# Kernel tuning notes

Measured on AMD Instinct MI355X. Metric: run time of the kernel, lower is better.

The kernel has to match this reference:

```python
import jax, jax.numpy as jnp
import numpy as np

B, A, V, D = 16, 1024, 512, 512
TEMPERATURE = 1.0
NEG = jnp.float32(-1e30)  # stand-in for -inf (avoids inf-inf NaNs in grads)
EPS = 1e-12               # F.normalize eps


def setup_inputs() -> dict:
    key = jax.random.key(0)
    k1, k2, k3 = jax.random.split(key, 3)
    audio_features = jax.random.normal(k1, (B, A, D), jnp.float32)
    video_features = jax.random.normal(k2, (B, V, D), jnp.float32)
    W = jax.random.normal(k3, (D, D), jnp.float32) / np.sqrt(D)  # nn.Linear weight [out,in]
    b = jnp.zeros((D,), jnp.float32)
    return {"audio_features": audio_features, "video_features": video_features, "W": W, "b": b}


def _normalize(x):
    n = jnp.linalg.norm(x, axis=-1, keepdims=True)
    return x / jnp.maximum(n, EPS)


def _dtw_score(sim):
    # sim: [B, A, V]. dp[i,j] = sim[i-1,j-1] + max(dp[i-1,j], dp[i,j-1], dp[i-1,j-1]).
    Bn, An, Vn = sim.shape
    init_row = jnp.full((Bn, Vn + 1), NEG).at[:, 0].set(0.0)  # dp row 0

    def row_step(prev_row, cost_row):
        # prev_row: [B, V+1], cost_row: [B, V]
        def col_step(left, xs):
            c, up, diag = xs  # each [B]
            val = c + jnp.maximum(jnp.maximum(up, left), diag)
            return val, val

        xs = (cost_row.T, prev_row[:, 1:].T, prev_row[:, :-1].T)  # [V, B] each
        _, vals = jax.lax.scan(col_step, jnp.full((Bn,), NEG), xs)  # vals: [V, B]
        new_row = jnp.concatenate([jnp.full((Bn, 1), NEG), vals.T], axis=1)
        return new_row, None

    final_row, _ = jax.lax.scan(row_step, init_row, jnp.swapaxes(sim, 0, 1))
    return final_row[:, -1]  # dp[:, A, V]


def reference(audio_features, video_features, W, b):
    audio_proj = jnp.einsum('bad,ed->bae', audio_features, W) + b
    video_proj = jnp.einsum('bvd,ed->bve', video_features, W) + b
    a_n = _normalize(audio_proj)
    v_n = _normalize(video_proj)
    similarity = jnp.einsum('bad,bvd->bav', a_n, v_n) / TEMPERATURE  # [B, A, V]
    alignment_score = _dtw_score(similarity)                          # [B]
    path_prob = jax.nn.softmax(similarity, axis=-1)
    aligned_video = jnp.einsum('bav,bvd->bad', path_prob, video_features)  # [B, A, D]
    return aligned_video, alignment_score
```

## Files before the change

### kernel.cpp

```cpp
#include <hip/hip_runtime.h>
#include <math.h>

#define B_DIM 16
#define A_DIM 1024
#define V_DIM 512
#define D_DIM 512
#define NEGV  (-1e30f)

typedef short bf16x8 __attribute__((ext_vector_type(8)));
typedef float floatx4 __attribute__((ext_vector_type(4)));

__device__ __forceinline__ short bf16_rne(float f) {
    unsigned u = __float_as_uint(f);
    return (short)((u + 0x7fffu + ((u >> 16) & 1u)) >> 16);
}

__device__ __forceinline__ float max3f(float a, float b, float c) {
    float d;
    asm("v_max3_f32 %0, %1, %2, %3" : "=v"(d) : "v"(a), "v"(b), "v"(c));
    return d;
}

__global__ __launch_bounds__(256) void cvt3_bf16_kernel(
    const float* __restrict__ in0, unsigned short* __restrict__ out0, int nb0,
    const float* __restrict__ in1, unsigned short* __restrict__ out1, int nb1,
    const float* __restrict__ in2, unsigned short* __restrict__ out2)
{
    int blk = blockIdx.x;
    const float* in; unsigned short* out;
    if (blk < nb0)              { in = in0; out = out0; }
    else if (blk < nb0 + nb1)   { in = in1; out = out1; blk -= nb0; }
    else                        { in = in2; out = out2; blk -= nb0 + nb1; }
    const int i = blk * 256 + threadIdx.x;
    float4 u = ((const float4*)in)[2*i];
    float4 v = ((const float4*)in)[2*i + 1];
    bf16x8 h;
    h[0]=bf16_rne(u.x); h[1]=bf16_rne(u.y); h[2]=bf16_rne(u.z); h[3]=bf16_rne(u.w);
    h[4]=bf16_rne(v.x); h[5]=bf16_rne(v.y); h[6]=bf16_rne(v.z); h[7]=bf16_rne(v.w);
    *(bf16x8*)(out + (size_t)i * 8) = h;
}

__global__ __launch_bounds__(256) void gemm_bf16_nt(
    const unsigned short* __restrict__ Ag, const unsigned short* __restrict__ Bg,
    const float* __restrict__ bias, float* __restrict__ Cg,
    int M, int N, int K, size_t strA, size_t strB, size_t strC)
{
    __shared__ __align__(16) unsigned short lA[8*64*8];
    __shared__ __align__(16) unsigned short lB[8*64*8];

    const unsigned short* Ab = Ag + (size_t)blockIdx.z * strA;
    const unsigned short* Bb = Bg + (size_t)blockIdx.z * strB;
    float*                Cb = Cg + (size_t)blockIdx.z * strC;

    const int m0 = blockIdx.y * 128;
    const int n0 = blockIdx.x * 128;
    const int tid = threadIdx.x, lane = tid & 63;
    const int w = tid >> 6, wy = w >> 1, wx = w & 1;

    const int u0 = tid, u1 = tid + 256;
    const int r_u0 = ((u0 >> 6) << 4) + (u0 & 15), k_u0 = ((u0 >> 4) & 3) * 8;
    const int r_u1 = ((u1 >> 6) << 4) + (u1 & 15), k_u1 = ((u1 >> 4) & 3) * 8;

    const unsigned short* gA0 = Ab + (size_t)(m0 + r_u0) * K + k_u0;
    const unsigned short* gA1 = Ab + (size_t)(m0 + r_u1) * K + k_u1;
    const unsigned short* gB0 = Bb + (size_t)(n0 + r_u0) * K + k_u0;
    const unsigned short* gB1 = Bb + (size_t)(n0 + r_u1) * K + k_u1;

    floatx4 acc[4][4];
    #pragma unroll
    for (int i = 0; i < 4; ++i)
        #pragma unroll
        for (int j = 0; j < 4; ++j) acc[i][j] = (floatx4){0.f, 0.f, 0.f, 0.f};

    bf16x8 a0 = *(const bf16x8*)(gA0);
    bf16x8 a1 = *(const bf16x8*)(gA1);
    bf16x8 b0 = *(const bf16x8*)(gB0);
    bf16x8 b1 = *(const bf16x8*)(gB1);

    for (int k0 = 0; k0 < K; k0 += 32) {
        __syncthreads();
        *(bf16x8*)&lA[(size_t)u0 * 8] = a0;
        *(bf16x8*)&lA[(size_t)u1 * 8] = a1;
        *(bf16x8*)&lB[(size_t)u0 * 8] = b0;
        *(bf16x8*)&lB[(size_t)u1 * 8] = b1;
        __syncthreads();

        if (k0 + 32 < K) {
            a0 = *(const bf16x8*)(gA0 + k0 + 32);
            a1 = *(const bf16x8*)(gA1 + k0 + 32);
            b0 = *(const bf16x8*)(gB0 + k0 + 32);
            b1 = *(const bf16x8*)(gB1 + k0 + 32);
        }

        bf16x8 fa[4], fb[4];
        #pragma unroll
        for (int t = 0; t < 4; ++t) {
            fa[t] = *(const bf16x8*)&lA[(((wy*4 + t)*64) + lane) * 8];
            fb[t] = *(const bf16x8*)&lB[(((wx*4 + t)*64) + lane) * 8];
        }
        #pragma unroll
        for (int i = 0; i < 4; ++i)
            #pragma unroll
            for (int j = 0; j < 4; ++j)
                acc[i][j] = __builtin_amdgcn_mfma_f32_16x16x32_bf16(fa[i], fb[j], acc[i][j], 0, 0, 0);
    }

    const int q = lane >> 4, c = lane & 15;
    #pragma unroll
    for (int i = 0; i < 4; ++i)
        #pragma unroll
        for (int j = 0; j < 4; ++j) {
            const int n = n0 + (wx*4 + j)*16 + c;
            const float bv = bias ? bias[n] : 0.f;
            #pragma unroll
            for (int r = 0; r < 4; ++r) {
                const int m = m0 + (wy*4 + i)*16 + q*4 + r;
                Cb[(size_t)m * N + n] = acc[i][j][r] + bv;
            }
        }
}

__global__ __launch_bounds__(256) void rownorm_cvt_kernel(
    const float* __restrict__ in, unsigned short* __restrict__ out)
{
    const int wave = threadIdx.x >> 6;
    const int lane = threadIdx.x & 63;
    const size_t r = (size_t)blockIdx.x * 4 + wave;
    const float* p = in + r * D_DIM + lane * 8;
    float4 u = *(const float4*)p;
    float4 w = *(const float4*)(p + 4);
    float ss = u.x*u.x + u.y*u.y + u.z*u.z + u.w*u.w
             + w.x*w.x + w.y*w.y + w.z*w.z + w.w*w.w;
    #pragma unroll
    for (int m = 1; m < 64; m <<= 1) ss += __shfl_xor(ss, m, 64);
    const float inv = 1.0f / fmaxf(sqrtf(ss), 1e-12f);
    bf16x8 h;
    h[0]=bf16_rne(u.x*inv); h[1]=bf16_rne(u.y*inv); h[2]=bf16_rne(u.z*inv); h[3]=bf16_rne(u.w*inv);
    h[4]=bf16_rne(w.x*inv); h[5]=bf16_rne(w.y*inv); h[6]=bf16_rne(w.z*inv); h[7]=bf16_rne(w.w*inv);
    *(bf16x8*)(out + r * D_DIM + lane * 8) = h;
}

template <int CTRL, int RMASK>
__device__ __forceinline__ float fdpp(float oldv, float src) {
    int r = __builtin_amdgcn_update_dpp(
        __float_as_int(oldv), __float_as_int(src), CTRL, RMASK, 0xF, false);
    return __int_as_float(r);
}

__global__ __launch_bounds__(256) void softmax_skew_kernel(
    const float* __restrict__ sim, unsigned short* __restrict__ Pbf,
    float* __restrict__ skew)
{
    const int wave = threadIdx.x >> 6;
    const int lane = threadIdx.x & 63;
    const size_t r = (size_t)blockIdx.x * 4 + wave;
    const float* p = sim + r * V_DIM + lane * 8;
    float4 u = *(const float4*)p;
    float4 w = *(const float4*)(p + 4);
    float s[8] = {u.x,u.y,u.z,u.w,w.x,w.y,w.z,w.w};

    float m = s[0];
    #pragma unroll
    for (int k = 1; k < 8; ++k) m = fmaxf(m, s[k]);
    #pragma unroll
    for (int t = 1; t < 64; t <<= 1) m = fmaxf(m, __shfl_xor(m, t, 64));

    const float L2E = 1.44269504f;
    float ex[8];
    float e = 0.f;
    #pragma unroll
    for (int k = 0; k < 8; ++k) { ex[k] = exp2f((s[k] - m) * L2E); e += ex[k]; }
    #pragma unroll
    for (int t = 1; t < 64; t <<= 1) e += __shfl_xor(e, t, 64);
    const float ri = 1.0f / e;

    bf16x8 h;
    #pragma unroll
    for (int k = 0; k < 8; ++k) h[k] = bf16_rne(ex[k] * ri);
    *(bf16x8*)(Pbf + r * V_DIM + lane * 8) = h;

    const int g  = ((int)r & 1023) >> 2;
    const int sh = (g & 63) + 72 * (g >> 6);
    float* Sk = skew + r * V_DIM;
    const int base = lane * 8 + sh;
    #pragma unroll
    for (int k = 0; k < 8; ++k) Sk[(base + k) & 511] = s[k];
}

__global__ __launch_bounds__(256) void transpose_cvt_kernel(
    const float* __restrict__ in, unsigned short* __restrict__ out)
{
    __shared__ float t[32][33];
    const int b = blockIdx.z;
    const int v0 = blockIdx.y * 32, d0 = blockIdx.x * 32;
    const int x = threadIdx.x & 31, y0 = (threadIdx.x >> 5) * 4;
    const float* I = in + ((size_t)b * V_DIM + v0) * D_DIM + d0;
    #pragma unroll
    for (int r = 0; r < 4; ++r) t[y0 + r][x] = I[(size_t)(y0 + r) * D_DIM + x];
    __syncthreads();
    unsigned short* O = out + ((size_t)b * D_DIM + d0) * V_DIM + v0;
    #pragma unroll
    for (int r = 0; r < 4; ++r) O[(size_t)(y0 + r) * V_DIM + x] = (unsigned short)bf16_rne(t[x][y0 + r]);
}

__global__ __launch_bounds__(256) void pv_dtw_kernel(
    const unsigned short* __restrict__ Pbf, const unsigned short* __restrict__ vTb,
    const float* __restrict__ skew, float* __restrict__ out_aligned,
    float* __restrict__ out_score)
{
    __shared__ __align__(16) unsigned short lA[8*64*8];
    __shared__ __align__(16) unsigned short lB[8*64*8];

    if (blockIdx.x < 16) {
        const int b    = blockIdx.x;
        const int tid  = threadIdx.x;
        const int lane = tid & 63;
        const int wv   = tid >> 6;
        const int off  = lane + 72 * wv;

        float* bndAll = (float*)lA;
        float* bndP = bndAll + wv * 520;
        const float* bndC = bndAll + (wv > 0 ? wv - 1 : 0) * 520;
        for (int i = tid; i < 3 * 520; i += 256) bndAll[i] = NEGV;
        __syncthreads();

        const float* R0 = skew + ((size_t)(b * 1024 + tid * 4)) * 512;
        const float* R1 = R0 + 512;
        const float* R2 = R0 + 1024;
        const float* R3 = R0 + 1536;

        float dp[4] = {NEGV, NEGV, NEGV, NEGV};
        float st[8];
        float upC = NEGV;
        float upL = (tid == 0) ? 0.0f : NEGV;

        float4 A0[4], A1[4], B0[4], B1[4];
        A0[0] = *(const float4*)(R0);      A1[0] = *(const float4*)(R0 + 4);
        A0[1] = *(const float4*)(R1);      A1[1] = *(const float4*)(R1 + 4);
        A0[2] = *(const float4*)(R2);      A1[2] = *(const float4*)(R2 + 4);
        A0[3] = *(const float4*)(R3);      A1[3] = *(const float4*)(R3 + 4);
        B0[0] = *(const float4*)(R0 + 8);  B1[0] = *(const float4*)(R0 + 12);
        B0[1] = *(const float4*)(R1 + 8);  B1[1] = *(const float4*)(R1 + 12);
        B0[2] = *(const float4*)(R2 + 8);  B1[2] = *(const float4*)(R2 + 12);
        B0[3] = *(const float4*)(R3 + 8);  B1[3] = *(const float4*)(R3 + 12);

#define DTW_STEP(K, CV0, CV1, CV2, CV3, FK)                                   \
        {                                                                     \
            const unsigned jj = (unsigned)(sb + (K) - off);                   \
            if (jj < 512u) {                                                  \
                float u = upC, g = upL, old, nd;                              \
                old = dp[0]; nd = (CV0) + max3f(u, dp[0], g); dp[0] = nd; g = old; u = nd; \
                old = dp[1]; nd = (CV1) + max3f(u, dp[1], g); dp[1] = nd; g = old; u = nd; \
                old = dp[2]; nd = (CV2) + max3f(u, dp[2], g); dp[2] = nd; g = old; u = nd; \
                old = dp[3]; nd = (CV3) + max3f(u, dp[3], g); dp[3] = nd;                  \
            }                                                                 \
            st[K] = dp[3];                                                    \
            upL = upC;                                                        \
            upC = fdpp<0x138, 0xF>((FK), dp[3]);                              \
        }

#define DTW_BATCH(C0, C1)                                                     \
        {                                                                     \
            float4 f0, f1;                                                    \
            const int ps = sb + 8 - 72 * wv;                                  \
            if (wv > 0 && ps >= 0 && ps <= 512) {                             \
                f0 = *(const float4*)&bndC[ps];                               \
                f1 = *(const float4*)&bndC[ps + 4];                           \
            } else {                                                          \
                f0 = make_float4(NEGV, NEGV, NEGV, NEGV); f1 = f0;            \
            }                                                                 \
            DTW_STEP(0, C0[0].x, C0[1].x, C0[2].x, C0[3].x, f0.x)             \
            DTW_STEP(1, C0[0].y, C0[1].y, C0[2].y, C0[3].y, f0.y)             \
            DTW_STEP(2, C0[0].z, C0[1].z, C0[2].z, C0[3].z, f0.z)             \
            DTW_STEP(3, C0[0].w, C0[1].w, C0[2].w, C0[3].w, f0.w)             \
            DTW_STEP(4, C1[0].x, C1[1].x, C1[2].x, C1[3].x, f1.x)             \
            DTW_STEP(5, C1[0].y, C1[1].y, C1[2].y, C1[3].y, f1.y)             \
            DTW_STEP(6, C1[0].z, C1[1].z, C1[2].z, C1[3].z, f1.z)             \
            DTW_STEP(7, C1[0].w, C1[1].w, C1[2].w, C1[3].w, f1.w)             \
            {                                                                 \
                const int o16 = (sb + 16) & 511;                              \
                C0[0] = *(const float4*)(R0 + o16); C1[0] = *(const float4*)(R0 + o16 + 4); \
                C0[1] = *(const float4*)(R1 + o16); C1[1] = *(const float4*)(R1 + o16 + 4); \
                C0[2] = *(const float4*)(R2 + o16); C1[2] = *(const float4*)(R2 + o16 + 4); \
                C0[3] = *(const float4*)(R3 + o16); C1[3] = *(const float4*)(R3 + o16 + 4); \
            }                                                                 \
            if (wv < 3 && lane == 63) {                                       \
                _Pragma("unroll")                                             \
                for (int k = 0; k < 8; ++k) {                                 \
                    const int jp = sb + k - 63 - 72 * wv;                     \
                    const int adr = ((unsigned)jp < 512u) ? (jp + 7) : 519;   \
                    bndP[adr] = st[k];                                        \
                }                                                             \
            }                                                                 \
            asm volatile("s_waitcnt lgkmcnt(0)" ::: "memory");                \
            __builtin_amdgcn_s_barrier();                                     \
            asm volatile("" ::: "memory");                                    \
        }

        #pragma unroll 1
        for (int bt = 0; bt < 100; bt += 2) {
            int sb = bt * 8;
            DTW_BATCH(A0, A1)
            sb += 8;
            DTW_BATCH(B0, B1)
        }
#undef DTW_BATCH
#undef DTW_STEP
        if (tid == 255) out_score[b] = dp[3];
        return;
    }

    const int bid = blockIdx.x - 16;
    const int n0 = (bid & 3) * 128;
    const int m0 = ((bid >> 2) & 7) * 128;
    const int bz = bid >> 5;
    const int K = V_DIM, N = D_DIM;

    const unsigned short* Ab = Pbf + (size_t)bz * A_DIM * V_DIM;
    const unsigned short* Bb = vTb + (size_t)bz * V_DIM * D_DIM;
    float*                Cb = out_aligned + (size_t)bz * A_DIM * D_DIM;

    const int tid = threadIdx.x, lane = tid & 63;
    const int w = tid >> 6, wy = w >> 1, wx = w & 1;
    const int u0 = tid, u1 = tid + 256;
    const int r_u0 = ((u0 >> 6) << 4) + (u0 & 15), k_u0 = ((u0 >> 4) & 3) * 8;
    const int r_u1 = ((u1 >> 6) << 4) + (u1 & 15), k_u1 = ((u1 >> 4) & 3) * 8;

    const unsigned short* gA0 = Ab + (size_t)(m0 + r_u0) * K + k_u0;
    const unsigned short* gA1 = Ab + (size_t)(m0 + r_u1) * K + k_u1;
    const unsigned short* gB0 = Bb + (size_t)(n0 + r_u0) * K + k_u0;
    const unsigned short* gB1 = Bb + (size_t)(n0 + r_u1) * K + k_u1;

    floatx4 acc[4][4];
    #pragma unroll
    for (int i = 0; i < 4; ++i)
        #pragma unroll
        for (int j = 0; j < 4; ++j) acc[i][j] = (floatx4){0.f, 0.f, 0.f, 0.f};

    bf16x8 a0 = *(const bf16x8*)(gA0);
    bf16x8 a1 = *(const bf16x8*)(gA1);
    bf16x8 b0 = *(const bf16x8*)(gB0);
    bf16x8 b1 = *(const bf16x8*)(gB1);

    for (int k0 = 0; k0 < K; k0 += 32) {
        __syncthreads();
        *(bf16x8*)&lA[(size_t)u0 * 8] = a0;
        *(bf16x8*)&lA[(size_t)u1 * 8] = a1;
        *(bf16x8*)&lB[(size_t)u0 * 8] = b0;
        *(bf16x8*)&lB[(size_t)u1 * 8] = b1;
        __syncthreads();
        if (k0 + 32 < K) {
            a0 = *(const bf16x8*)(gA0 + k0 + 32);
            a1 = *(const bf16x8*)(gA1 + k0 + 32);
            b0 = *(const bf16x8*)(gB0 + k0 + 32);
            b1 = *(const bf16x8*)(gB1 + k0 + 32);
        }
        bf16x8 fa[4], fb[4];
        #pragma unroll
        for (int t = 0; t < 4; ++t) {
            fa[t] = *(const bf16x8*)&lA[(((wy*4 + t)*64) + lane) * 8];
            fb[t] = *(const bf16x8*)&lB[(((wx*4 + t)*64) + lane) * 8];
        }
        #pragma unroll
        for (int i = 0; i < 4; ++i)
            #pragma unroll
            for (int j = 0; j < 4; ++j)
                acc[i][j] = __builtin_amdgcn_mfma_f32_16x16x32_bf16(fa[i], fb[j], acc[i][j], 0, 0, 0);
    }

    const int q = lane >> 4, c = lane & 15;
    #pragma unroll
    for (int i = 0; i < 4; ++i)
        #pragma unroll
        for (int j = 0; j < 4; ++j) {
            const int n = n0 + (wx*4 + j)*16 + c;
            #pragma unroll
            for (int r = 0; r < 4; ++r) {
                const int m = m0 + (wy*4 + i)*16 + q*4 + r;
                Cb[(size_t)m * N + n] = acc[i][j][r];
            }
        }
}

extern "C" void kernel_launch(void* const* d_in, const int* in_sizes, int n_in,
                              void* d_out, int out_size, void* d_ws, size_t ws_size,
                              hipStream_t stream)
{
    const float* audio = (const float*)d_in[0];
    const float* video = (const float*)d_in[1];
    const float* W     = (const float*)d_in[2];
    const float* bias  = (const float*)d_in[3];

    float* out_aligned = (float*)d_out;
    float* out_score   = (float*)d_out + (size_t)B_DIM * A_DIM * D_DIM;

    const size_t NA = (size_t)B_DIM * A_DIM * D_DIM;
    const size_t NV = (size_t)B_DIM * V_DIM * D_DIM;
    const size_t NS = (size_t)B_DIM * A_DIM * V_DIM;

    float* ws = (float*)d_ws;
    float*          a_p  = ws;
    float*          v_p  = a_p + NA;
    float*          sim  = v_p + NV;
    unsigned short* abf  = (unsigned short*)(sim + NS);
    unsigned short* vbf  = (unsigned short*)(sim + NS) + NA;
    unsigned short* v_nb = vbf + NV;
    unsigned short* Wbf  = v_nb + NV;
    unsigned short* a_nb = (unsigned short*)v_p;
    unsigned short* Pbf  = abf;
    unsigned short* vTb  = vbf;
    float*          skew = a_p;

    {
        const int nb_a = (int)(NA / 8 / 256);
        const int nb_v = (int)(NV / 8 / 256);
        const int nb_w = D_DIM * D_DIM / 8 / 256;
        cvt3_bf16_kernel<<<dim3(nb_a + nb_v + nb_w), dim3(256), 0, stream>>>(
            audio, abf, nb_a, video, vbf, nb_v, W, Wbf);
    }

    gemm_bf16_nt<<<dim3(D_DIM/128, (B_DIM*A_DIM)/128, 1), dim3(256), 0, stream>>>(
        abf, Wbf, bias, a_p, B_DIM*A_DIM, D_DIM, D_DIM, 0, 0, 0);
    gemm_bf16_nt<<<dim3(D_DIM/128, (B_DIM*V_DIM)/128, 1), dim3(256), 0, stream>>>(
        vbf, Wbf, bias, v_p, B_DIM*V_DIM, D_DIM, D_DIM, 0, 0, 0);

    rownorm_cvt_kernel<<<dim3((B_DIM*V_DIM)/4), dim3(256), 0, stream>>>(v_p, v_nb);
    rownorm_cvt_kernel<<<dim3((B_DIM*A_DIM)/4), dim3(256), 0, stream>>>(a_p, a_nb);

    gemm_bf16_nt<<<dim3(V_DIM/128, A_DIM/128, B_DIM), dim3(256), 0, stream>>>(
        a_nb, v_nb, nullptr, sim, A_DIM, V_DIM, D_DIM,
        (size_t)A_DIM*D_DIM, (size_t)V_DIM*D_DIM, (size_t)A_DIM*V_DIM);

    transpose_cvt_kernel<<<dim3(D_DIM/32, V_DIM/32, B_DIM), dim3(256), 0, stream>>>(video, vTb);

    softmax_skew_kernel<<<dim3((B_DIM*A_DIM)/4), dim3(256), 0, stream>>>(sim, Pbf, skew);

    pv_dtw_kernel<<<dim3(16 + (D_DIM/128)*(A_DIM/128)*B_DIM), dim3(256), 0, stream>>>(
        Pbf, vTb, skew, out_aligned, out_score);
}
```

Before: 324.6 us.

## Transpose DTW cost layout for coalesced loads and merge projection/norm launches

Softmax now writes a column-major, skewed copy of the similarity matrix through shared memory. Each DTW thread then fetches four consecutive rows with one coalesced float4 per diagonal step instead of strided row reads. The two projection GEMMs are merged into one launch, and the two row-norm kernels plus the video transpose are merged into another, which reduces launch count and tail effects. A shared GEMM tile body is factored out. The skewed buffer is wider (768 columns), so there are extra writes, and softmax gains a shared-memory transpose step.

```diff
diff --git a/kernel.cpp b/kernel.cpp
--- a/kernel.cpp
+++ b/kernel.cpp
@@ -6,6 +6,7 @@
 #define V_DIM 512
 #define D_DIM 512
 #define NEGV  (-1e30f)
+#define SKT_W 768
 
 typedef short bf16x8 __attribute__((ext_vector_type(8)));
 typedef float floatx4 __attribute__((ext_vector_type(4)));
@@ -40,20 +41,12 @@
     *(bf16x8*)(out + (size_t)i * 8) = h;
 }
 
-__global__ __launch_bounds__(256) void gemm_bf16_nt(
-    const unsigned short* __restrict__ Ag, const unsigned short* __restrict__ Bg,
-    const float* __restrict__ bias, float* __restrict__ Cg,
-    int M, int N, int K, size_t strA, size_t strB, size_t strC)
-{
-    __shared__ __align__(16) unsigned short lA[8*64*8];
-    __shared__ __align__(16) unsigned short lB[8*64*8];
-
-    const unsigned short* Ab = Ag + (size_t)blockIdx.z * strA;
-    const unsigned short* Bb = Bg + (size_t)blockIdx.z * strB;
-    float*                Cb = Cg + (size_t)blockIdx.z * strC;
-
-    const int m0 = blockIdx.y * 128;
-    const int n0 = blockIdx.x * 128;
+__device__ __forceinline__ void gemm_tile_body(
+    const unsigned short* __restrict__ Ab, const unsigned short* __restrict__ Bb,
+    const float* __restrict__ bias, float* __restrict__ Cb,
+    int m0, int n0, int K, int N,
+    unsigned short* lA, unsigned short* lB)
+{
     const int tid = threadIdx.x, lane = tid & 63;
     const int w = tid >> 6, wy = w >> 1, wx = w & 1;
 
@@ -120,24 +113,73 @@
         }
 }
 
-__global__ __launch_bounds__(256) void rownorm_cvt_kernel(
-    const float* __restrict__ in, unsigned short* __restrict__ out)
-{
-    const int wave = threadIdx.x >> 6;
-    const int lane = threadIdx.x & 63;
-    const size_t r = (size_t)blockIdx.x * 4 + wave;
-    const float* p = in + r * D_DIM + lane * 8;
-    float4 u = *(const float4*)p;
-    float4 w = *(const float4*)(p + 4);
-    float ss = u.x*u.x + u.y*u.y + u.z*u.z + u.w*u.w
-             + w.x*w.x + w.y*w.y + w.z*w.z + w.w*w.w;
-    #pragma unroll
-    for (int m = 1; m < 64; m <<= 1) ss += __shfl_xor(ss, m, 64);
-    const float inv = 1.0f / fmaxf(sqrtf(ss), 1e-12f);
-    bf16x8 h;
-    h[0]=bf16_rne(u.x*inv); h[1]=bf16_rne(u.y*inv); h[2]=bf16_rne(u.z*inv); h[3]=bf16_rne(u.w*inv);
-    h[4]=bf16_rne(w.x*inv); h[5]=bf16_rne(w.y*inv); h[6]=bf16_rne(w.z*inv); h[7]=bf16_rne(w.w*inv);
-    *(bf16x8*)(out + r * D_DIM + lane * 8) = h;
+__global__ __launch_bounds__(256) void gemm_bf16_nt(
+    const unsigned short* __restrict__ Ag, const unsigned short* __restrict__ Bg,
+    const float* __restrict__ bias, float* __restrict__ Cg,
+    int M, int N, int K, size_t strA, size_t strB, size_t strC)
+{
+    __shared__ __align__(16) unsigned short lA[8*64*8];
+    __shared__ __align__(16) unsigned short lB[8*64*8];
+    const unsigned short* Ab = Ag + (size_t)blockIdx.z * strA;
+    const unsigned short* Bb = Bg + (size_t)blockIdx.z * strB;
+    float*                Cb = Cg + (size_t)blockIdx.z * strC;
+    gemm_tile_body(Ab, Bb, bias, Cb, blockIdx.y * 128, blockIdx.x * 128, K, N, lA, lB);
+}
+
+__global__ __launch_bounds__(256) void gemm_proj2(
+    const unsigned short* __restrict__ abf, const unsigned short* __restrict__ vbf,
+    const unsigned short* __restrict__ Wbf, const float* __restrict__ bias,
+    float* __restrict__ a_p, float* __restrict__ v_p)
+{
+    __shared__ __align__(16) unsigned short lA[8*64*8];
+    __shared__ __align__(16) unsigned short lB[8*64*8];
+    const int by = blockIdx.y;
+    const unsigned short* Ab; float* Cb; int m0;
+    if (by < 128) { Ab = abf; Cb = a_p; m0 = by * 128; }
+    else          { Ab = vbf; Cb = v_p; m0 = (by - 128) * 128; }
+    gemm_tile_body(Ab, Wbf, bias, Cb, m0, blockIdx.x * 128, D_DIM, D_DIM, lA, lB);
+}
+
+__global__ __launch_bounds__(256) void norm2_transpose_kernel(
+    const float* __restrict__ a_p, unsigned short* __restrict__ a_nb,
+    const float* __restrict__ v_p, unsigned short* __restrict__ v_nb,
+    const float* __restrict__ video, unsigned short* __restrict__ vTb)
+{
+    __shared__ float t[32][33];
+    const int bx = blockIdx.x;
+    if (bx < 6144) {
+        const float* in; unsigned short* out; int rb;
+        if (bx < 4096) { in = a_p; out = a_nb; rb = bx; }
+        else           { in = v_p; out = v_nb; rb = bx - 4096; }
+        const int wave = threadIdx.x >> 6;
+        const int lane = threadIdx.x & 63;
+        const size_t r = (size_t)rb * 4 + wave;
+        const float* p = in + r * D_DIM + lane * 8;
+        float4 u = *(const float4*)p;
+        float4 w = *(const float4*)(p + 4);
+        float ss = u.x*u.x + u.y*u.y + u.z*u.z + u.w*u.w
+                 + w.x*w.x + w.y*w.y + w.z*w.z + w.w*w.w;
+        #pragma unroll
+        for (int m = 1; m < 64; m <<= 1) ss += __shfl_xor(ss, m, 64);
+        const float inv = 1.0f / fmaxf(sqrtf(ss), 1e-12f);
+        bf16x8 h;
+        h[0]=bf16_rne(u.x*inv); h[1]=bf16_rne(u.y*inv); h[2]=bf16_rne(u.z*inv); h[3]=bf16_rne(u.w*inv);
+        h[4]=bf16_rne(w.x*inv); h[5]=bf16_rne(w.y*inv); h[6]=bf16_rne(w.z*inv); h[7]=bf16_rne(w.w*inv);
+        *(bf16x8*)(out + r * D_DIM + lane * 8) = h;
+    } else {
+        const int tt = bx - 6144;
+        const int d0 = (tt & 15) * 32;
+        const int v0 = ((tt >> 4) & 15) * 32;
+        const int b  = tt >> 8;
+        const int x = threadIdx.x & 31, y0 = (threadIdx.x >> 5) * 4;
+        const float* I = video + ((size_t)b * V_DIM + v0) * D_DIM + d0;
+        #pragma unroll
+        for (int r = 0; r < 4; ++r) t[y0 + r][x] = I[(size_t)(y0 + r) * D_DIM + x];
+        __syncthreads();
+        unsigned short* O = vTb + ((size_t)b * D_DIM + d0) * V_DIM + v0;
+        #pragma unroll
+        for (int r = 0; r < 4; ++r) O[(size_t)(y0 + r) * V_DIM + x] = (unsigned short)bf16_rne(t[x][y0 + r]);
+    }
 }
 
 template <int CTRL, int RMASK>
@@ -147,10 +189,11 @@
     return __int_as_float(r);
 }
 
-__global__ __launch_bounds__(256) void softmax_skew_kernel(
+__global__ __launch_bounds__(256) void softmax_skewT_kernel(
     const float* __restrict__ sim, unsigned short* __restrict__ Pbf,
-    float* __restrict__ skew)
-{
+    float* __restrict__ skewT)
+{
+    __shared__ float tl[4][520];
     const int wave = threadIdx.x >> 6;
     const int lane = threadIdx.x & 63;
     const size_t r = (size_t)blockIdx.x * 4 + wave;
@@ -179,33 +222,28 @@
     for (int k = 0; k < 8; ++k) h[k] = bf16_rne(ex[k] * ri);
     *(bf16x8*)(Pbf + r * V_DIM + lane * 8) = h;
 
-    const int g  = ((int)r & 1023) >> 2;
-    const int sh = (g & 63) + 72 * (g >> 6);
-    float* Sk = skew + r * V_DIM;
-    const int base = lane * 8 + sh;
-    #pragma unroll
-    for (int k = 0; k < 8; ++k) Sk[(base + k) & 511] = s[k];
-}
-
-__global__ __launch_bounds__(256) void transpose_cvt_kernel(
-    const float* __restrict__ in, unsigned short* __restrict__ out)
-{
-    __shared__ float t[32][33];
-    const int b = blockIdx.z;
-    const int v0 = blockIdx.y * 32, d0 = blockIdx.x * 32;
-    const int x = threadIdx.x & 31, y0 = (threadIdx.x >> 5) * 4;
-    const float* I = in + ((size_t)b * V_DIM + v0) * D_DIM + d0;
-    #pragma unroll
-    for (int r = 0; r < 4; ++r) t[y0 + r][x] = I[(size_t)(y0 + r) * D_DIM + x];
+    #pragma unroll
+    for (int k = 0; k < 8; ++k) tl[wave][lane * 8 + k] = s[k];
     __syncthreads();
-    unsigned short* O = out + ((size_t)b * D_DIM + d0) * V_DIM + v0;
-    #pragma unroll
-    for (int r = 0; r < 4; ++r) O[(size_t)(y0 + r) * V_DIM + x] = (unsigned short)bf16_rne(t[x][y0 + r]);
+
+    const int r0 = blockIdx.x * 4;
+    const int b  = r0 >> 10;
+    const int i0 = r0 & 1023;
+    const int g  = i0 >> 2;
+    const int off = (g & 63) + 72 * (g >> 6);
+    float* sbase = skewT + (size_t)b * SKT_W * 1024 + i0;
+    #pragma unroll
+    for (int cc = 0; cc < 2; ++cc) {
+        const int c = threadIdx.x + cc * 256;
+        int pc = c + off; if (pc >= SKT_W) pc -= SKT_W;
+        float4 v = make_float4(tl[0][c], tl[1][c], tl[2][c], tl[3][c]);
+        *(float4*)(sbase + (size_t)pc * 1024) = v;
+    }
 }
 
 __global__ __launch_bounds__(256) void pv_dtw_kernel(
     const unsigned short* __restrict__ Pbf, const unsigned short* __restrict__ vTb,
-    const float* __restrict__ skew, float* __restrict__ out_aligned,
+    const float* __restrict__ skewT, float* __restrict__ out_aligned,
     float* __restrict__ out_score)
 {
     __shared__ __align__(16) unsigned short lA[8*64*8];
@@ -224,42 +262,35 @@
         for (int i = tid; i < 3 * 520; i += 256) bndAll[i] = NEGV;
         __syncthreads();
 
-        const float* R0 = skew + ((size_t)(b * 1024 + tid * 4)) * 512;
-        const float* R1 = R0 + 512;
-        const float* R2 = R0 + 1024;
-        const float* R3 = R0 + 1536;
+        const float* Sb = skewT + (size_t)b * SKT_W * 1024 + 4 * tid;
 
         float dp[4] = {NEGV, NEGV, NEGV, NEGV};
         float st[8];
         float upC = NEGV;
         float upL = (tid == 0) ? 0.0f : NEGV;
 
-        float4 A0[4], A1[4], B0[4], B1[4];
-        A0[0] = *(const float4*)(R0);      A1[0] = *(const float4*)(R0 + 4);
-        A0[1] = *(const float4*)(R1);      A1[1] = *(const float4*)(R1 + 4);
-        A0[2] = *(const float4*)(R2);      A1[2] = *(const float4*)(R2 + 4);
-        A0[3] = *(const float4*)(R3);      A1[3] = *(const float4*)(R3 + 4);
-        B0[0] = *(const float4*)(R0 + 8);  B1[0] = *(const float4*)(R0 + 12);
-        B0[1] = *(const float4*)(R1 + 8);  B1[1] = *(const float4*)(R1 + 12);
-        B0[2] = *(const float4*)(R2 + 8);  B1[2] = *(const float4*)(R2 + 12);
-        B0[3] = *(const float4*)(R3 + 8);  B1[3] = *(const float4*)(R3 + 12);
-
-#define DTW_STEP(K, CV0, CV1, CV2, CV3, FK)                                   \
+        float4 CA[8], CB[8];
+        #pragma unroll
+        for (int k = 0; k < 8; ++k) CA[k] = *(const float4*)(Sb + (size_t)k * 1024);
+        #pragma unroll
+        for (int k = 0; k < 8; ++k) CB[k] = *(const float4*)(Sb + (size_t)(k + 8) * 1024);
+
+#define DTW_STEP(K, CK, FK)                                                   \
         {                                                                     \
             const unsigned jj = (unsigned)(sb + (K) - off);                   \
             if (jj < 512u) {                                                  \
                 float u = upC, g = upL, old, nd;                              \
-                old = dp[0]; nd = (CV0) + max3f(u, dp[0], g); dp[0] = nd; g = old; u = nd; \
-                old = dp[1]; nd = (CV1) + max3f(u, dp[1], g); dp[1] = nd; g = old; u = nd; \
-                old = dp[2]; nd = (CV2) + max3f(u, dp[2], g); dp[2] = nd; g = old; u = nd; \
-                old = dp[3]; nd = (CV3) + max3f(u, dp[3], g); dp[3] = nd;                  \
+                old = dp[0]; nd = (CK).x + max3f(u, dp[0], g); dp[0] = nd; g = old; u = nd; \
+                old = dp[1]; nd = (CK).y + max3f(u, dp[1], g); dp[1] = nd; g = old; u = nd; \
+                old = dp[2]; nd = (CK).z + max3f(u, dp[2], g); dp[2] = nd; g = old; u = nd; \
+                old = dp[3]; nd = (CK).w + max3f(u, dp[3], g); dp[3] = nd;                  \
             }                                                                 \
             st[K] = dp[3];                                                    \
             upL = upC;                                                        \
             upC = fdpp<0x138, 0xF>((FK), dp[3]);                              \
         }
 
-#define DTW_BATCH(C0, C1)                                                     \
+#define DTW_BATCH(CC)                                                         \
         {                                                                     \
             float4 f0, f1;                                                    \
             const int ps = sb + 8 - 72 * wv;                                  \
@@ -269,20 +300,16 @@
             } else {                                                          \
                 f0 = make_float4(NEGV, NEGV, NEGV, NEGV); f1 = f0;            \
             }                                                                 \
-            DTW_STEP(0, C0[0].x, C0[1].x, C0[2].x, C0[3].x, f0.x)             \
-            DTW_STEP(1, C0[0].y, C0[1].y, C0[2].y, C0[3].y, f0.y)             \
-            DTW_STEP(2, C0[0].z, C0[1].z, C0[2].z, C0[3].z, f0.z)             \
-            DTW_STEP(3, C0[0].w, C0[1].w, C0[2].w, C0[3].w, f0.w)             \
-            DTW_STEP(4, C1[0].x, C1[1].x, C1[2].x, C1[3].x, f1.x)             \
-            DTW_STEP(5, C1[0].y, C1[1].y, C1[2].y, C1[3].y, f1.y)             \
-            DTW_STEP(6, C1[0].z, C1[1].z, C1[2].z, C1[3].z, f1.z)             \
-            DTW_STEP(7, C1[0].w, C1[1].w, C1[2].w, C1[3].w, f1.w)             \
+            DTW_STEP(0, CC[0], f0.x) DTW_STEP(1, CC[1], f0.y)                 \
+            DTW_STEP(2, CC[2], f0.z) DTW_STEP(3, CC[3], f0.w)                 \
+            DTW_STEP(4, CC[4], f1.x) DTW_STEP(5, CC[5], f1.y)                 \
+            DTW_STEP(6, CC[6], f1.z) DTW_STEP(7, CC[7], f1.w)                 \
             {                                                                 \
-                const int o16 = (sb + 16) & 511;                              \
-                C0[0] = *(const float4*)(R0 + o16); C1[0] = *(const float4*)(R0 + o16 + 4); \
-                C0[1] = *(const float4*)(R1 + o16); C1[1] = *(const float4*)(R1 + o16 + 4); \
-                C0[2] = *(const float4*)(R2 + o16); C1[2] = *(const float4*)(R2 + o16 + 4); \
-                C0[3] = *(const float4*)(R3 + o16); C1[3] = *(const float4*)(R3 + o16 + 4); \
+                _Pragma("unroll")                                             \
+                for (int k = 0; k < 8; ++k) {                                 \
+                    int cc_ = sb + 16 + k; if (cc_ >= SKT_W) cc_ -= SKT_W;    \
+                    CC[k] = *(const float4*)(Sb + (size_t)cc_ * 1024);        \
+                }                                                             \
             }                                                                 \
             if (wv < 3 && lane == 63) {                                       \
                 _Pragma("unroll")                                             \
@@ -300,9 +327,9 @@
         #pragma unroll 1
         for (int bt = 0; bt < 100; bt += 2) {
             int sb = bt * 8;
-            DTW_BATCH(A0, A1)
+            DTW_BATCH(CA)
             sb += 8;
-            DTW_BATCH(B0, B1)
+            DTW_BATCH(CB)
         }
 #undef DTW_BATCH
 #undef DTW_STEP
@@ -314,72 +341,12 @@
     const int n0 = (bid & 3) * 128;
     const int m0 = ((bid >> 2) & 7) * 128;
     const int bz = bid >> 5;
-    const int K = V_DIM, N = D_DIM;
 
     const unsigned short* Ab = Pbf + (size_t)bz * A_DIM * V_DIM;
     const unsigned short* Bb = vTb + (size_t)bz * V_DIM * D_DIM;
     float*                Cb = out_aligned + (size_t)bz * A_DIM * D_DIM;
 
-    const int tid = threadIdx.x, lane = tid & 63;
-    const int w = tid >> 6, wy = w >> 1, wx = w & 1;
-    const int u0 = tid, u1 = tid + 256;
-    const int r_u0 = ((u0 >> 6) << 4) + (u0 & 15), k_u0 = ((u0 >> 4) & 3) * 8;
-    const int r_u1 = ((u1 >> 6) << 4) + (u1 & 15), k_u1 = ((u1 >> 4) & 3) * 8;
-
-    const unsigned short* gA0 = Ab + (size_t)(m0 + r_u0) * K + k_u0;
-    const unsigned short* gA1 = Ab + (size_t)(m0 + r_u1) * K + k_u1;
-    const unsigned short* gB0 = Bb + (size_t)(n0 + r_u0) * K + k_u0;
-    const unsigned short* gB1 = Bb + (size_t)(n0 + r_u1) * K + k_u1;
-
-    floatx4 acc[4][4];
-    #pragma unroll
-    for (int i = 0; i < 4; ++i)
-        #pragma unroll
-        for (int j = 0; j < 4; ++j) acc[i][j] = (floatx4){0.f, 0.f, 0.f, 0.f};
-
-    bf16x8 a0 = *(const bf16x8*)(gA0);
-    bf16x8 a1 = *(const bf16x8*)(gA1);
-    bf16x8 b0 = *(const bf16x8*)(gB0);
-    bf16x8 b1 = *(const bf16x8*)(gB1);
-
-    for (int k0 = 0; k0 < K; k0 += 32) {
-        __syncthreads();
-        *(bf16x8*)&lA[(size_t)u0 * 8] = a0;
-        *(bf16x8*)&lA[(size_t)u1 * 8] = a1;
-        *(bf16x8*)&lB[(size_t)u0 * 8] = b0;
-        *(bf16x8*)&lB[(size_t)u1 * 8] = b1;
-        __syncthreads();
-        if (k0 + 32 < K) {
-            a0 = *(const bf16x8*)(gA0 + k0 + 32);
-            a1 = *(const bf16x8*)(gA1 + k0 + 32);
-            b0 = *(const bf16x8*)(gB0 + k0 + 32);
-            b1 = *(const bf16x8*)(gB1 + k0 + 32);
-        }
-        bf16x8 fa[4], fb[4];
-        #pragma unroll
-        for (int t = 0; t < 4; ++t) {
-            fa[t] = *(const bf16x8*)&lA[(((wy*4 + t)*64) + lane) * 8];
-            fb[t] = *(const bf16x8*)&lB[(((wx*4 + t)*64) + lane) * 8];
-        }
-        #pragma unroll
-        for (int i = 0; i < 4; ++i)
-            #pragma unroll
-            for (int j = 0; j < 4; ++j)
-                acc[i][j] = __builtin_amdgcn_mfma_f32_16x16x32_bf16(fa[i], fb[j], acc[i][j], 0, 0, 0);
-    }
-
-    const int q = lane >> 4, c = lane & 15;
-    #pragma unroll
-    for (int i = 0; i < 4; ++i)
-        #pragma unroll
-        for (int j = 0; j < 4; ++j) {
-            const int n = n0 + (wx*4 + j)*16 + c;
-            #pragma unroll
-            for (int r = 0; r < 4; ++r) {
-                const int m = m0 + (wy*4 + i)*16 + q*4 + r;
-                Cb[(size_t)m * N + n] = acc[i][j][r];
-            }
-        }
+    gemm_tile_body(Ab, Bb, nullptr, Cb, m0, n0, V_DIM, D_DIM, lA, lB);
 }
 
 extern "C" void kernel_launch(void* const* d_in, const int* in_sizes, int n_in,
@@ -406,10 +373,10 @@
     unsigned short* vbf  = (unsigned short*)(sim + NS) + NA;
     unsigned short* v_nb = vbf + NV;
     unsigned short* Wbf  = v_nb + NV;
-    unsigned short* a_nb = (unsigned short*)v_p;
+    unsigned short* a_nb = abf;
     unsigned short* Pbf  = abf;
     unsigned short* vTb  = vbf;
-    float*          skew = a_p;
+    float*          skewT = a_p;
 
     {
         const int nb_a = (int)(NA / 8 / 256);
@@ -419,22 +386,18 @@
             audio, abf, nb_a, video, vbf, nb_v, W, Wbf);
     }
 
-    gemm_bf16_nt<<<dim3(D_DIM/128, (B_DIM*A_DIM)/128, 1), dim3(256), 0, stream>>>(
-        abf, Wbf, bias, a_p, B_DIM*A_DIM, D_DIM, D_DIM, 0, 0, 0);
-    gemm_bf16_nt<<<dim3(D_DIM/128, (B_DIM*V_DIM)/128, 1), dim3(256), 0, stream>>>(
-        vbf, Wbf, bias, v_p, B_DIM*V_DIM, D_DIM, D_DIM, 0, 0, 0);
-
-    rownorm_cvt_kernel<<<dim3((B_DIM*V_DIM)/4), dim3(256), 0, stream>>>(v_p, v_nb);
-    rownorm_cvt_kernel<<<dim3((B_DIM*A_DIM)/4), dim3(256), 0, stream>>>(a_p, a_nb);
+    gemm_proj2<<<dim3(D_DIM/128, 192), dim3(256), 0, stream>>>(
+        abf, vbf, Wbf, bias, a_p, v_p);
+
+    norm2_transpose_kernel<<<dim3(4096 + 2048 + 4096), dim3(256), 0, stream>>>(
+        a_p, a_nb, v_p, v_nb, video, vTb);
 
     gemm_bf16_nt<<<dim3(V_DIM/128, A_DIM/128, B_DIM), dim3(256), 0, stream>>>(
         a_nb, v_nb, nullptr, sim, A_DIM, V_DIM, D_DIM,
         (size_t)A_DIM*D_DIM, (size_t)V_DIM*D_DIM, (size_t)A_DIM*V_DIM);
 
-    transpose_cvt_kernel<<<dim3(D_DIM/32, V_DIM/32, B_DIM), dim3(256), 0, stream>>>(video, vTb);
-
-    softmax_skew_kernel<<<dim3((B_DIM*A_DIM)/4), dim3(256), 0, stream>>>(sim, Pbf, skew);
+    softmax_skewT_kernel<<<dim3((B_DIM*A_DIM)/4), dim3(256), 0, stream>>>(sim, Pbf, skewT);
 
     pv_dtw_kernel<<<dim3(16 + (D_DIM/128)*(A_DIM/128)*B_DIM), dim3(256), 0, stream>>>(
-        Pbf, vTb, skew, out_aligned, out_score);
-}
+        Pbf, vTb, skewT, out_aligned, out_score);
+}
```

Result: faster. 284.5 us (-12.4%).
